# Optimization experiments

Hardware: AMD Instinct MI355X
Metric: run time of the kernel (lower is better)

The kernel has to match this reference:

```python
import jax, jax.numpy as jnp
import numpy as np

B, H, S, D = 2, 16, 2048, 64


def setup_inputs() -> dict:
    key = jax.random.key(0)
    kq, kk, kv = jax.random.split(key, 3)
    queries = jax.random.normal(kq, (B, H, S, D), dtype=jnp.float32)
    keys = jax.random.normal(kk, (B, H, S, D), dtype=jnp.float32)
    values = jax.random.normal(kv, (B, H, S, D), dtype=jnp.float32)
    scaling_factor = jnp.asarray(np.sqrt(D), dtype=jnp.float32)
    # causal mask, broadcast over heads: True = attend
    causal = jnp.tril(jnp.ones((S, S), dtype=bool))
    mask = jnp.broadcast_to(causal[None, None, :, :], (B, 1, S, S))
    return {
        "queries": queries,
        "keys": keys,
        "values": values,
        "scaling_factor": scaling_factor,
        "mask": mask,
    }


def reference(queries, keys, values, scaling_factor, mask):
    # scores: [B, H, S, S]
    scores = jnp.einsum("bhqd,bhkd->bhqk", queries, keys) / scaling_factor
    scores = jnp.where(mask, scores, -jnp.inf)
    attn = jax.nn.softmax(scores, axis=-1)
    # embeddings: [B, H, S, D]
    return jnp.einsum("bhqk,bhkd->bhqd", attn, values)
```

## Files before the change

### kernel.cpp

```cpp
#include <hip/hip_runtime.h>
#include <hip/hip_bf16.h>


typedef __attribute__((ext_vector_type(8))) short bf16x8;
typedef __attribute__((ext_vector_type(4))) float f32x4;
typedef unsigned uint2v __attribute__((ext_vector_type(2)));

#define MFMA32K(a, b, c) __builtin_amdgcn_mfma_f32_16x16x32_bf16(a, b, c, 0, 0, 0)

constexpr int Bsz = 2, Hn = 16, Sn = 2048, Dn = 64;
constexpr int QBLK = 64, KBLK = 64;
constexpr int NE = Bsz * Hn * Sn * Dn;

#if defined(__has_builtin)
#if __has_builtin(__builtin_amdgcn_exp2f)
#define EXP2(x) __builtin_amdgcn_exp2f(x)
#endif
#endif
#ifndef EXP2
#define EXP2(x) exp2f(x)
#endif

__device__ inline short f2bf(float f) {
  union { float f; unsigned u; } v;
  v.f = f;
  unsigned r = v.u + 0x7FFF + ((v.u >> 16) & 1);
  return (short)(r >> 16);
}

__device__ inline unsigned pk_bf16(float lo, float hi) {
  unsigned r;
  asm("v_cvt_pk_bf16_f32 %0, %1, %2" : "=v"(r) : "v"(lo), "v"(hi));
  return r;
}

__device__ inline void gl2lds16(const void* g, void* l) {
  __builtin_amdgcn_global_load_lds(
      (const __attribute__((address_space(1))) unsigned int*)g,
      (__attribute__((address_space(3))) unsigned int*)l, 16, 0, 0);
}

__device__ inline int swz(int row, int colbyte) {
  return row * 128 + (colbyte ^ ((row & 7) << 4));
}

#if defined(__has_builtin)
#if __has_builtin(__builtin_amdgcn_permlane16_swap) && \
    __has_builtin(__builtin_amdgcn_permlane32_swap)
#define HAVE_PERMLANE_SWAP 1
#endif
#endif

__device__ inline float xred_max(float x) {
#ifdef HAVE_PERMLANE_SWAP
  uint2v a = __builtin_amdgcn_permlane16_swap(__float_as_uint(x),
                                              __float_as_uint(x), false, false);
  x = fmaxf(__uint_as_float(a[0]), __uint_as_float(a[1]));
  uint2v b = __builtin_amdgcn_permlane32_swap(__float_as_uint(x),
                                              __float_as_uint(x), false, false);
  x = fmaxf(__uint_as_float(b[0]), __uint_as_float(b[1]));
#else
  x = fmaxf(x, __shfl_xor(x, 16, 64));
  x = fmaxf(x, __shfl_xor(x, 32, 64));
#endif
  return x;
}

__global__ __launch_bounds__(256) void prep(const float* __restrict__ K,
                                            const float* __restrict__ V,
                                            short* __restrict__ Kb,
                                            short* __restrict__ Vt) {
  const int tile = blockIdx.x, bh = blockIdx.y;
  const int tid = threadIdx.x;
  const int r = tid >> 2, c = (tid & 3) * 16;
  const size_t base = (size_t)bh * Sn * Dn;

  if (blockIdx.z == 0) {
    const float* kp = K + base + (size_t)(tile * 64 + r) * Dn + c;
    float4 x0 = *(const float4*)(kp + 0);
    float4 x1 = *(const float4*)(kp + 4);
    float4 x2 = *(const float4*)(kp + 8);
    float4 x3 = *(const float4*)(kp + 12);
    bf16x8 w0, w1;
    w0[0] = f2bf(x0.x); w0[1] = f2bf(x0.y); w0[2] = f2bf(x0.z); w0[3] = f2bf(x0.w);
    w0[4] = f2bf(x1.x); w0[5] = f2bf(x1.y); w0[6] = f2bf(x1.z); w0[7] = f2bf(x1.w);
    w1[0] = f2bf(x2.x); w1[1] = f2bf(x2.y); w1[2] = f2bf(x2.z); w1[3] = f2bf(x2.w);
    w1[4] = f2bf(x3.x); w1[5] = f2bf(x3.y); w1[6] = f2bf(x3.z); w1[7] = f2bf(x3.w);
    short* op = Kb + base + (size_t)(tile * 64 + r) * Dn + c;
    *(bf16x8*)op = w0;
    *(bf16x8*)(op + 8) = w1;
  } else {
    __shared__ short t[64][66];
    const float* vp = V + base + (size_t)(tile * 64 + r) * Dn + c;
    float4 x0 = *(const float4*)(vp + 0);
    float4 x1 = *(const float4*)(vp + 4);
    float4 x2 = *(const float4*)(vp + 8);
    float4 x3 = *(const float4*)(vp + 12);
    short* tr = &t[r][c];
    tr[0] = f2bf(x0.x); tr[1] = f2bf(x0.y); tr[2] = f2bf(x0.z); tr[3] = f2bf(x0.w);
    tr[4] = f2bf(x1.x); tr[5] = f2bf(x1.y); tr[6] = f2bf(x1.z); tr[7] = f2bf(x1.w);
    tr[8] = f2bf(x2.x); tr[9] = f2bf(x2.y); tr[10] = f2bf(x2.z); tr[11] = f2bf(x2.w);
    tr[12] = f2bf(x3.x); tr[13] = f2bf(x3.y); tr[14] = f2bf(x3.z); tr[15] = f2bf(x3.w);
    __syncthreads();
    short* op = Vt + base + (size_t)r * Sn + tile * 64 + c;
    bf16x8 w0, w1;
#pragma unroll
    for (int j = 0; j < 8; ++j) {
      int p0 = c + j, p1 = c + 8 + j;
      int k0 = 32 * (p0 >> 5) + 16 * ((p0 >> 2) & 1) + 4 * ((p0 >> 3) & 3) + (p0 & 3);
      int k1 = 32 * (p1 >> 5) + 16 * ((p1 >> 2) & 1) + 4 * ((p1 >> 3) & 3) + (p1 & 3);
      w0[j] = t[k0][r];
      w1[j] = t[k1][r];
    }
    *(bf16x8*)op = w0;
    *(bf16x8*)(op + 8) = w1;
  }
}

__global__ __launch_bounds__(256, 4) void attn_fwd(
    const float* __restrict__ Q, const short* __restrict__ Kb,
    const short* __restrict__ Vt, const float* __restrict__ SF,
    float* __restrict__ O) {
  __shared__ short Kbuf[2][64 * 64];
  __shared__ short Vbuf[2][64 * 64];

  const int bh = blockIdx.x;
  const int qt = (gridDim.y - 1) - blockIdx.y;
  const int tid = threadIdx.x;
  const int wave = tid >> 6, lane = tid & 63;
  const int g = lane >> 4, lc = lane & 15;
  const float qscale = 1.4426950408889634f / SF[0];

  const size_t base = (size_t)bh * Sn * Dn;
  const int qg = qt * QBLK + wave * 16 + lc;

  int ka[4][2], va[2][4];
#pragma unroll
  for (int t = 0; t < 4; ++t) {
    ka[t][0] = swz(t * 16 + lc, g * 16);
    ka[t][1] = swz(t * 16 + lc, g * 16 + 64);
  }
#pragma unroll
  for (int t2 = 0; t2 < 2; ++t2)
#pragma unroll
    for (int dt = 0; dt < 4; ++dt)
      va[t2][dt] = swz(dt * 16 + lc, t2 * 64 + g * 16);
  int koff[2], voff[2];
#pragma unroll
  for (int j = 0; j < 2; ++j) {
    int c = wave * 2 + j;
    int off = c * 1024 + lane * 16;
    int row = off >> 7;
    int col = (off & 127) ^ ((row & 7) << 4);
    koff[j] = row * 128 + col;
    voff[j] = row * (Sn * 2) + col;
  }

  const char* kpg = (const char*)(Kb + base);
  const char* vpg = (const char*)(Vt + base);

  auto stageK = [&](int buf) {
#pragma unroll
    for (int j = 0; j < 2; ++j)
      gl2lds16(kpg + koff[j], (char*)Kbuf[buf] + (wave * 2 + j) * 1024);
    kpg += KBLK * Dn * 2;
  };
  auto stageV = [&](int buf) {
#pragma unroll
    for (int j = 0; j < 2; ++j)
      gl2lds16(vpg + voff[j], (char*)Vbuf[buf] + (wave * 2 + j) * 1024);
    vpg += KBLK * 2;
  };

  bf16x8 bq[2];
  {
    const float* qp = Q + base + (size_t)qg * Dn + g * 8;
#pragma unroll
    for (int h = 0; h < 2; ++h) {
      float4 x0 = *(const float4*)(qp + 32 * h);
      float4 x1 = *(const float4*)(qp + 32 * h + 4);
      bf16x8 a;
      a[0] = f2bf(x0.x * qscale); a[1] = f2bf(x0.y * qscale);
      a[2] = f2bf(x0.z * qscale); a[3] = f2bf(x0.w * qscale);
      a[4] = f2bf(x1.x * qscale); a[5] = f2bf(x1.y * qscale);
      a[6] = f2bf(x1.z * qscale); a[7] = f2bf(x1.w * qscale);
      bq[h] = a;
    }
  }

  bf16x8 ones;
#pragma unroll
  for (int j = 0; j < 8; ++j) ones[j] = (short)0x3F80;

  f32x4 o[4], lsum = (f32x4){0.f, 0.f, 0.f, 0.f};
#pragma unroll
  for (int dt = 0; dt < 4; ++dt) o[dt] = (f32x4){0.f, 0.f, 0.f, 0.f};
  float m = -10000.0f;

  const int nt = qt + 1;
  int cur = 0;
  stageK(0);
  stageV(0);
  __syncthreads();

  for (int kt = 0; kt < nt; ++kt) {
    if (kt + 1 < nt) { stageK(cur ^ 1); stageV(cur ^ 1); }

    const char* Kc = (const char*)Kbuf[cur];
    const char* Vc = (const char*)Vbuf[cur];

    f32x4 s[4];
    __builtin_amdgcn_s_setprio(1);
#pragma unroll
    for (int t = 0; t < 4; ++t) {
      bf16x8 ak0 = *(const bf16x8*)(Kc + ka[t][0]);
      bf16x8 ak1 = *(const bf16x8*)(Kc + ka[t][1]);
      f32x4 z = (f32x4){0.f, 0.f, 0.f, 0.f};
      z = MFMA32K(ak0, bq[0], z);
      z = MFMA32K(ak1, bq[1], z);
      s[t] = z;
    }
    __builtin_amdgcn_s_setprio(0);

    if (kt == qt) {
      const int kb = kt * KBLK;
#pragma unroll
      for (int t = 0; t < 4; ++t)
#pragma unroll
        for (int i = 0; i < 4; ++i) {
          int kg = kb + t * 16 + g * 4 + i;
          if (kg > qg) s[t][i] = -30000.0f;
        }
    }

    float pmax = fmaxf(fmaxf(s[0][0], s[0][1]), fmaxf(s[0][2], s[0][3]));
#pragma unroll
    for (int t = 1; t < 4; ++t)
      pmax = fmaxf(pmax, fmaxf(fmaxf(s[t][0], s[t][1]),
                               fmaxf(s[t][2], s[t][3])));
    pmax = xred_max(pmax);
    if (!__all(pmax - m <= 8.0f)) {
      float mnew = fmaxf(m, pmax);
      float alpha = EXP2(m - mnew);
      lsum[0] *= alpha;
#pragma unroll
      for (int dt = 0; dt < 4; ++dt) o[dt] *= alpha;
      m = mnew;
    }
#pragma unroll
    for (int t = 0; t < 4; ++t)
#pragma unroll
      for (int i = 0; i < 4; ++i) s[t][i] = EXP2(s[t][i] - m);

    union { unsigned uu[4]; bf16x8 v; } pb[2];
#pragma unroll
    for (int t2 = 0; t2 < 2; ++t2) {
      pb[t2].uu[0] = pk_bf16(s[2 * t2][0], s[2 * t2][1]);
      pb[t2].uu[1] = pk_bf16(s[2 * t2][2], s[2 * t2][3]);
      pb[t2].uu[2] = pk_bf16(s[2 * t2 + 1][0], s[2 * t2 + 1][1]);
      pb[t2].uu[3] = pk_bf16(s[2 * t2 + 1][2], s[2 * t2 + 1][3]);
    }
    __builtin_amdgcn_s_setprio(1);
#pragma unroll
    for (int t2 = 0; t2 < 2; ++t2) {
      lsum = MFMA32K(ones, pb[t2].v, lsum);
#pragma unroll
      for (int dt = 0; dt < 4; ++dt) {
        bf16x8 av = *(const bf16x8*)(Vc + va[t2][dt]);
        o[dt] = MFMA32K(av, pb[t2].v, o[dt]);
      }
    }
    __builtin_amdgcn_s_setprio(0);

    __syncthreads();
    cur ^= 1;
  }

  const float inv = 1.0f / lsum[0];
  float* op = O + base + (size_t)qg * Dn;
#pragma unroll
  for (int dt = 0; dt < 4; ++dt) {
    f32x4 r = o[dt] * inv;
    *(f32x4*)(op + dt * 16 + g * 4) = r;
  }
}

extern "C" void kernel_launch(void* const* d_in, const int* in_sizes, int n_in,
                              void* d_out, int out_size, void* d_ws, size_t ws_size,
                              hipStream_t stream) {
  const float* Q = (const float*)d_in[0];
  const float* K = (const float*)d_in[1];
  const float* V = (const float*)d_in[2];
  const float* SF = (const float*)d_in[3];
  float* O = (float*)d_out;

  short* Kb = (short*)d_ws;
  short* Vt = Kb + NE;

  prep<<<dim3(Sn / 64, Bsz * Hn, 2), 256, 0, stream>>>(K, V, Kb, Vt);
  attn_fwd<<<dim3(Bsz * Hn, Sn / QBLK), 256, 0, stream>>>(Q, Kb, Vt, SF, O);
}
```

Before: 50.34 us.

## Pair causal query tiles per block and load V fragments directly from global

Each block now handles two query tiles (qt and 31-qt) one after the other, so every block does the same amount of causal work, and the grid is halved. V is no longer staged through LDS; each lane reads its V fragments straight from global memory into registers at the start of each iteration. Launch bounds drop to 2 blocks per CU, which allows more registers. The trade-off is fewer blocks in flight, global-latency V loads sitting on the critical path, and extra register pressure from holding the V fragments.

```diff
diff --git a/kernel.cpp b/kernel.cpp
--- a/kernel.cpp
+++ b/kernel.cpp
@@ -117,63 +117,51 @@
   }
 }
 
-__global__ __launch_bounds__(256, 4) void attn_fwd(
+__global__ __launch_bounds__(256, 2) void attn_fwd(
     const float* __restrict__ Q, const short* __restrict__ Kb,
     const short* __restrict__ Vt, const float* __restrict__ SF,
     float* __restrict__ O) {
   __shared__ short Kbuf[2][64 * 64];
-  __shared__ short Vbuf[2][64 * 64];
 
   const int bh = blockIdx.x;
-  const int qt = (gridDim.y - 1) - blockIdx.y;
+  const int py = blockIdx.y;
+  const int qtA = 31 - py, qtB = py;
+  const int nA = qtA + 1, nTot = nA + qtB + 1;
+
   const int tid = threadIdx.x;
   const int wave = tid >> 6, lane = tid & 63;
   const int g = lane >> 4, lc = lane & 15;
   const float qscale = 1.4426950408889634f / SF[0];
 
   const size_t base = (size_t)bh * Sn * Dn;
-  const int qg = qt * QBLK + wave * 16 + lc;
-
-  int ka[4][2], va[2][4];
+  const char* Kg = (const char*)(Kb + base);
+
+  int ka[4][2];
 #pragma unroll
   for (int t = 0; t < 4; ++t) {
     ka[t][0] = swz(t * 16 + lc, g * 16);
     ka[t][1] = swz(t * 16 + lc, g * 16 + 64);
   }
-#pragma unroll
-  for (int t2 = 0; t2 < 2; ++t2)
-#pragma unroll
-    for (int dt = 0; dt < 4; ++dt)
-      va[t2][dt] = swz(dt * 16 + lc, t2 * 64 + g * 16);
-  int koff[2], voff[2];
+  int koff[2];
 #pragma unroll
   for (int j = 0; j < 2; ++j) {
-    int c = wave * 2 + j;
-    int off = c * 1024 + lane * 16;
-    int row = off >> 7;
-    int col = (off & 127) ^ ((row & 7) << 4);
-    koff[j] = row * 128 + col;
-    voff[j] = row * (Sn * 2) + col;
-  }
-
-  const char* kpg = (const char*)(Kb + base);
-  const char* vpg = (const char*)(Vt + base);
-
-  auto stageK = [&](int buf) {
+    int c = (wave * 2 + j) * 1024 + lane * 16;
+    int row = c >> 7;
+    koff[j] = row * 128 + ((c & 127) ^ ((row & 7) << 4));
+  }
+  const char* vb[4];
+#pragma unroll
+  for (int dt = 0; dt < 4; ++dt)
+    vb[dt] = (const char*)(Vt + base) + (size_t)(dt * 16 + lc) * (Sn * 2) + g * 16;
+
+  auto stageK = [&](int kt, int buf) {
+    const char* src = Kg + ((size_t)kt << 13);
 #pragma unroll
     for (int j = 0; j < 2; ++j)
-      gl2lds16(kpg + koff[j], (char*)Kbuf[buf] + (wave * 2 + j) * 1024);
-    kpg += KBLK * Dn * 2;
+      gl2lds16(src + koff[j], (char*)Kbuf[buf] + (wave * 2 + j) * 1024);
   };
-  auto stageV = [&](int buf) {
-#pragma unroll
-    for (int j = 0; j < 2; ++j)
-      gl2lds16(vpg + voff[j], (char*)Vbuf[buf] + (wave * 2 + j) * 1024);
-    vpg += KBLK * 2;
-  };
-
-  bf16x8 bq[2];
-  {
+
+  auto loadQ = [&](int qg, bf16x8* bq) {
     const float* qp = Q + base + (size_t)qg * Dn + g * 8;
 #pragma unroll
     for (int h = 0; h < 2; ++h) {
@@ -186,28 +174,42 @@
       a[6] = f2bf(x1.z * qscale); a[7] = f2bf(x1.w * qscale);
       bq[h] = a;
     }
-  }
+  };
 
   bf16x8 ones;
 #pragma unroll
   for (int j = 0; j < 8; ++j) ones[j] = (short)0x3F80;
+
+  int qt = qtA;
+  int qg = qt * QBLK + wave * 16 + lc;
+  bf16x8 bq[2];
+  loadQ(qg, bq);
 
   f32x4 o[4], lsum = (f32x4){0.f, 0.f, 0.f, 0.f};
 #pragma unroll
   for (int dt = 0; dt < 4; ++dt) o[dt] = (f32x4){0.f, 0.f, 0.f, 0.f};
   float m = -10000.0f;
 
-  const int nt = qt + 1;
   int cur = 0;
-  stageK(0);
-  stageV(0);
+  stageK(0, 0);
   __syncthreads();
 
-  for (int kt = 0; kt < nt; ++kt) {
-    if (kt + 1 < nt) { stageK(cur ^ 1); stageV(cur ^ 1); }
+  for (int it = 0; it < nTot; ++it) {
+    const int kt = (it < nA) ? it : it - nA;
+
+    bf16x8 vf[2][4];
+#pragma unroll
+    for (int t2 = 0; t2 < 2; ++t2)
+#pragma unroll
+      for (int dt = 0; dt < 4; ++dt)
+        vf[t2][dt] = *(const bf16x8*)(vb[dt] + kt * 128 + t2 * 64);
+
+    if (it + 1 < nTot) {
+      int nkt = (it + 1 < nA) ? it + 1 : it + 1 - nA;
+      stageK(nkt, cur ^ 1);
+    }
 
     const char* Kc = (const char*)Kbuf[cur];
-    const char* Vc = (const char*)Vbuf[cur];
 
     f32x4 s[4];
     __builtin_amdgcn_s_setprio(1);
@@ -265,15 +267,30 @@
     for (int t2 = 0; t2 < 2; ++t2) {
       lsum = MFMA32K(ones, pb[t2].v, lsum);
 #pragma unroll
-      for (int dt = 0; dt < 4; ++dt) {
-        bf16x8 av = *(const bf16x8*)(Vc + va[t2][dt]);
-        o[dt] = MFMA32K(av, pb[t2].v, o[dt]);
-      }
+      for (int dt = 0; dt < 4; ++dt)
+        o[dt] = MFMA32K(vf[t2][dt], pb[t2].v, o[dt]);
     }
     __builtin_amdgcn_s_setprio(0);
 
     __syncthreads();
     cur ^= 1;
+
+    if (it == nA - 1) {
+      const float inv = 1.0f / lsum[0];
+      float* op = O + base + (size_t)qg * Dn;
+#pragma unroll
+      for (int dt = 0; dt < 4; ++dt) {
+        f32x4 r = o[dt] * inv;
+        *(f32x4*)(op + dt * 16 + g * 4) = r;
+      }
+      qt = qtB;
+      qg = qt * QBLK + wave * 16 + lc;
+      loadQ(qg, bq);
+#pragma unroll
+      for (int dt = 0; dt < 4; ++dt) o[dt] = (f32x4){0.f, 0.f, 0.f, 0.f};
+      lsum = (f32x4){0.f, 0.f, 0.f, 0.f};
+      m = -10000.0f;
+    }
   }
 
   const float inv = 1.0f / lsum[0];
@@ -298,5 +315,5 @@
   short* Vt = Kb + NE;
 
   prep<<<dim3(Sn / 64, Bsz * Hn, 2), 256, 0, stream>>>(K, V, Kb, Vt);
-  attn_fwd<<<dim3(Bsz * Hn, Sn / QBLK), 256, 0, stream>>>(Q, Kb, Vt, SF, O);
-}
+  attn_fwd<<<dim3(Bsz * Hn, 16), 256, 0, stream>>>(Q, Kb, Vt, SF, O);
+}
```

Result: slower. 81.99 us (+62.9%).

## Split KV tiles across wave pairs with 32-row queries per wave and merge

Applied to the files above, without the earlier changes.

Each attention block now gives every wave 32 query rows instead of 16, so each K/V fragment read from LDS feeds twice as many MFMAs. Waves are paired: one wave takes even KV tiles and the other takes odd tiles, and at the end the partial softmax states are merged through shared memory. The prep kernel now converts K and V in one block instead of two grid slices. In exchange, both LDS buffers hold different tiles at once, so each pair of tiles is loaded synchronously with two barriers and the overlap of loads with compute is lost. Register pressure also rises.

```diff
diff --git a/kernel.cpp b/kernel.cpp
--- a/kernel.cpp
+++ b/kernel.cpp
@@ -9,7 +9,7 @@
 #define MFMA32K(a, b, c) __builtin_amdgcn_mfma_f32_16x16x32_bf16(a, b, c, 0, 0, 0)
 
 constexpr int Bsz = 2, Hn = 16, Sn = 2048, Dn = 64;
-constexpr int QBLK = 64, KBLK = 64;
+constexpr int KBLK = 64;
 constexpr int NE = Bsz * Hn * Sn * Dn;
 
 #if defined(__has_builtin)
@@ -70,12 +70,13 @@
                                             const float* __restrict__ V,
                                             short* __restrict__ Kb,
                                             short* __restrict__ Vt) {
+  __shared__ short t[64][66];
   const int tile = blockIdx.x, bh = blockIdx.y;
   const int tid = threadIdx.x;
   const int r = tid >> 2, c = (tid & 3) * 16;
   const size_t base = (size_t)bh * Sn * Dn;
 
-  if (blockIdx.z == 0) {
+  {
     const float* kp = K + base + (size_t)(tile * 64 + r) * Dn + c;
     float4 x0 = *(const float4*)(kp + 0);
     float4 x1 = *(const float4*)(kp + 4);
@@ -89,8 +90,8 @@
     short* op = Kb + base + (size_t)(tile * 64 + r) * Dn + c;
     *(bf16x8*)op = w0;
     *(bf16x8*)(op + 8) = w1;
-  } else {
-    __shared__ short t[64][66];
+  }
+  {
     const float* vp = V + base + (size_t)(tile * 64 + r) * Dn + c;
     float4 x0 = *(const float4*)(vp + 0);
     float4 x1 = *(const float4*)(vp + 4);
@@ -128,11 +129,19 @@
   const int qt = (gridDim.y - 1) - blockIdx.y;
   const int tid = threadIdx.x;
   const int wave = tid >> 6, lane = tid & 63;
+  const int qh = wave >> 1, par = wave & 1;
   const int g = lane >> 4, lc = lane & 15;
   const float qscale = 1.4426950408889634f / SF[0];
 
   const size_t base = (size_t)bh * Sn * Dn;
-  const int qg = qt * QBLK + wave * 16 + lc;
+  const char* Kg = (const char*)(Kb + base);
+  const char* Vg = (const char*)(Vt + base);
+  const int nkv = qt + 1;
+  const int npairs = (nkv + 1) >> 1;
+
+  int qg[2];
+  qg[0] = qt * 64 + qh * 32 + lc;
+  qg[1] = qg[0] + 16;
 
   int ka[4][2], va[2][4];
 #pragma unroll
@@ -148,33 +157,30 @@
   int koff[2], voff[2];
 #pragma unroll
   for (int j = 0; j < 2; ++j) {
-    int c = wave * 2 + j;
-    int off = c * 1024 + lane * 16;
+    int off = (wave * 2 + j) * 1024 + lane * 16;
     int row = off >> 7;
     int col = (off & 127) ^ ((row & 7) << 4);
     koff[j] = row * 128 + col;
-    voff[j] = row * (Sn * 2) + col;
-  }
-
-  const char* kpg = (const char*)(Kb + base);
-  const char* vpg = (const char*)(Vt + base);
-
-  auto stageK = [&](int buf) {
+    voff[j] = row * 4096 + col;
+  }
+
+  auto stageK = [&](int kt, int buf) {
+    const char* src = Kg + (size_t)kt * 8192;
 #pragma unroll
     for (int j = 0; j < 2; ++j)
-      gl2lds16(kpg + koff[j], (char*)Kbuf[buf] + (wave * 2 + j) * 1024);
-    kpg += KBLK * Dn * 2;
+      gl2lds16(src + koff[j], (char*)Kbuf[buf] + (wave * 2 + j) * 1024);
   };
-  auto stageV = [&](int buf) {
+  auto stageV = [&](int kt, int buf) {
+    const char* src = Vg + (size_t)kt * 128;
 #pragma unroll
     for (int j = 0; j < 2; ++j)
-      gl2lds16(vpg + voff[j], (char*)Vbuf[buf] + (wave * 2 + j) * 1024);
-    vpg += KBLK * 2;
+      gl2lds16(src + voff[j], (char*)Vbuf[buf] + (wave * 2 + j) * 1024);
   };
 
-  bf16x8 bq[2];
-  {
-    const float* qp = Q + base + (size_t)qg * Dn + g * 8;
+  bf16x8 bq[2][2];
+#pragma unroll
+  for (int u = 0; u < 2; ++u) {
+    const float* qp = Q + base + (size_t)qg[u] * Dn + g * 8;
 #pragma unroll
     for (int h = 0; h < 2; ++h) {
       float4 x0 = *(const float4*)(qp + 32 * h);
@@ -184,7 +190,7 @@
       a[2] = f2bf(x0.z * qscale); a[3] = f2bf(x0.w * qscale);
       a[4] = f2bf(x1.x * qscale); a[5] = f2bf(x1.y * qscale);
       a[6] = f2bf(x1.z * qscale); a[7] = f2bf(x1.w * qscale);
-      bq[h] = a;
+      bq[u][h] = a;
     }
   }
 
@@ -192,96 +198,142 @@
 #pragma unroll
   for (int j = 0; j < 8; ++j) ones[j] = (short)0x3F80;
 
-  f32x4 o[4], lsum = (f32x4){0.f, 0.f, 0.f, 0.f};
-#pragma unroll
-  for (int dt = 0; dt < 4; ++dt) o[dt] = (f32x4){0.f, 0.f, 0.f, 0.f};
-  float m = -10000.0f;
-
-  const int nt = qt + 1;
-  int cur = 0;
-  stageK(0);
-  stageV(0);
+  f32x4 o[2][4], lsum[2];
+  float m[2] = {-10000.0f, -10000.0f};
+#pragma unroll
+  for (int u = 0; u < 2; ++u) {
+    lsum[u] = (f32x4){0.f, 0.f, 0.f, 0.f};
+#pragma unroll
+    for (int dt = 0; dt < 4; ++dt) o[u][dt] = (f32x4){0.f, 0.f, 0.f, 0.f};
+  }
+
+  stageK(0, 0);
+  stageV(0, 0);
+  if (nkv > 1) { stageK(1, 1); stageV(1, 1); }
   __syncthreads();
 
-  for (int kt = 0; kt < nt; ++kt) {
-    if (kt + 1 < nt) { stageK(cur ^ 1); stageV(cur ^ 1); }
-
-    const char* Kc = (const char*)Kbuf[cur];
-    const char* Vc = (const char*)Vbuf[cur];
-
-    f32x4 s[4];
-    __builtin_amdgcn_s_setprio(1);
-#pragma unroll
-    for (int t = 0; t < 4; ++t) {
-      bf16x8 ak0 = *(const bf16x8*)(Kc + ka[t][0]);
-      bf16x8 ak1 = *(const bf16x8*)(Kc + ka[t][1]);
-      f32x4 z = (f32x4){0.f, 0.f, 0.f, 0.f};
-      z = MFMA32K(ak0, bq[0], z);
-      z = MFMA32K(ak1, bq[1], z);
-      s[t] = z;
-    }
-    __builtin_amdgcn_s_setprio(0);
-
-    if (kt == qt) {
-      const int kb = kt * KBLK;
-#pragma unroll
-      for (int t = 0; t < 4; ++t)
-#pragma unroll
-        for (int i = 0; i < 4; ++i) {
-          int kg = kb + t * 16 + g * 4 + i;
-          if (kg > qg) s[t][i] = -30000.0f;
+  for (int j = 0; j < npairs; ++j) {
+    const int myt = 2 * j + par;
+    if (myt < nkv) {
+      const char* Kc = (const char*)Kbuf[par];
+      const char* Vc = (const char*)Vbuf[par];
+
+      f32x4 s[2][4];
+      __builtin_amdgcn_s_setprio(1);
+#pragma unroll
+      for (int t = 0; t < 4; ++t) {
+        bf16x8 ak0 = *(const bf16x8*)(Kc + ka[t][0]);
+        bf16x8 ak1 = *(const bf16x8*)(Kc + ka[t][1]);
+#pragma unroll
+        for (int u = 0; u < 2; ++u) {
+          f32x4 z = (f32x4){0.f, 0.f, 0.f, 0.f};
+          z = MFMA32K(ak0, bq[u][0], z);
+          z = MFMA32K(ak1, bq[u][1], z);
+          s[u][t] = z;
         }
-    }
-
-    float pmax = fmaxf(fmaxf(s[0][0], s[0][1]), fmaxf(s[0][2], s[0][3]));
-#pragma unroll
-    for (int t = 1; t < 4; ++t)
-      pmax = fmaxf(pmax, fmaxf(fmaxf(s[t][0], s[t][1]),
-                               fmaxf(s[t][2], s[t][3])));
-    pmax = xred_max(pmax);
-    if (!__all(pmax - m <= 8.0f)) {
-      float mnew = fmaxf(m, pmax);
-      float alpha = EXP2(m - mnew);
-      lsum[0] *= alpha;
-#pragma unroll
-      for (int dt = 0; dt < 4; ++dt) o[dt] *= alpha;
-      m = mnew;
-    }
-#pragma unroll
-    for (int t = 0; t < 4; ++t)
-#pragma unroll
-      for (int i = 0; i < 4; ++i) s[t][i] = EXP2(s[t][i] - m);
-
-    union { unsigned uu[4]; bf16x8 v; } pb[2];
-#pragma unroll
-    for (int t2 = 0; t2 < 2; ++t2) {
-      pb[t2].uu[0] = pk_bf16(s[2 * t2][0], s[2 * t2][1]);
-      pb[t2].uu[1] = pk_bf16(s[2 * t2][2], s[2 * t2][3]);
-      pb[t2].uu[2] = pk_bf16(s[2 * t2 + 1][0], s[2 * t2 + 1][1]);
-      pb[t2].uu[3] = pk_bf16(s[2 * t2 + 1][2], s[2 * t2 + 1][3]);
-    }
-    __builtin_amdgcn_s_setprio(1);
-#pragma unroll
-    for (int t2 = 0; t2 < 2; ++t2) {
-      lsum = MFMA32K(ones, pb[t2].v, lsum);
+      }
+      __builtin_amdgcn_s_setprio(0);
+
+      if (myt == qt) {
+        const int kb = myt * KBLK;
+#pragma unroll
+        for (int u = 0; u < 2; ++u)
+#pragma unroll
+          for (int t = 0; t < 4; ++t)
+#pragma unroll
+            for (int i = 0; i < 4; ++i) {
+              int kg = kb + t * 16 + g * 4 + i;
+              if (kg > qg[u]) s[u][t][i] = -30000.0f;
+            }
+      }
+
+      union { unsigned uu[4]; bf16x8 v; } pb[2][2];
+#pragma unroll
+      for (int u = 0; u < 2; ++u) {
+        float a0 = fmaxf(fmaxf(s[u][0][0], s[u][0][1]), s[u][0][2]);
+        float a1 = fmaxf(fmaxf(s[u][0][3], s[u][1][0]), s[u][1][1]);
+        float a2 = fmaxf(fmaxf(s[u][1][2], s[u][1][3]), s[u][2][0]);
+        float a3 = fmaxf(fmaxf(s[u][2][1], s[u][2][2]), s[u][2][3]);
+        float a4 = fmaxf(fmaxf(s[u][3][0], s[u][3][1]), s[u][3][2]);
+        float b0 = fmaxf(fmaxf(a0, a1), a2);
+        float b1 = fmaxf(fmaxf(a3, a4), s[u][3][3]);
+        float plocal = fmaxf(b0, b1);
+        if (!__all(plocal - m[u] <= 8.0f)) {
+          float pmax = xred_max(plocal);
+          float mnew = fmaxf(m[u], pmax);
+          float alpha = EXP2(m[u] - mnew);
+          lsum[u][0] *= alpha;
+#pragma unroll
+          for (int dt = 0; dt < 4; ++dt) o[u][dt] *= alpha;
+          m[u] = mnew;
+        }
+#pragma unroll
+        for (int t = 0; t < 4; ++t)
+#pragma unroll
+          for (int i = 0; i < 4; ++i) s[u][t][i] = EXP2(s[u][t][i] - m[u]);
+#pragma unroll
+        for (int t2 = 0; t2 < 2; ++t2) {
+          pb[u][t2].uu[0] = pk_bf16(s[u][2 * t2][0], s[u][2 * t2][1]);
+          pb[u][t2].uu[1] = pk_bf16(s[u][2 * t2][2], s[u][2 * t2][3]);
+          pb[u][t2].uu[2] = pk_bf16(s[u][2 * t2 + 1][0], s[u][2 * t2 + 1][1]);
+          pb[u][t2].uu[3] = pk_bf16(s[u][2 * t2 + 1][2], s[u][2 * t2 + 1][3]);
+        }
+      }
+
+      __builtin_amdgcn_s_setprio(1);
+#pragma unroll
+      for (int t2 = 0; t2 < 2; ++t2) {
+        lsum[0] = MFMA32K(ones, pb[0][t2].v, lsum[0]);
+        lsum[1] = MFMA32K(ones, pb[1][t2].v, lsum[1]);
+#pragma unroll
+        for (int dt = 0; dt < 4; ++dt) {
+          bf16x8 av = *(const bf16x8*)(Vc + va[t2][dt]);
+          o[0][dt] = MFMA32K(av, pb[0][t2].v, o[0][dt]);
+          o[1][dt] = MFMA32K(av, pb[1][t2].v, o[1][dt]);
+        }
+      }
+      __builtin_amdgcn_s_setprio(0);
+    }
+
+    __syncthreads();
+
+    const int nt0 = 2 * j + 2;
+    if (nt0 < nkv) { stageK(nt0, 0); stageV(nt0, 0); }
+    if (nt0 + 1 < nkv) { stageK(nt0 + 1, 1); stageV(nt0 + 1, 1); }
+    __syncthreads();
+  }
+
+  float* scr = (qh == 0) ? (float*)&Kbuf[0][0] : (float*)&Vbuf[0][0];
+  if (par == 1) {
+#pragma unroll
+    for (int u = 0; u < 2; ++u) {
+#pragma unroll
+      for (int dt = 0; dt < 4; ++dt)
+        *(f32x4*)(scr + (u * 16 + lc) * 64 + dt * 16 + g * 4) = o[u][dt];
+      if (g == 0) {
+        scr[2048 + u * 16 + lc] = m[u];
+        scr[2080 + u * 16 + lc] = lsum[u][0];
+      }
+    }
+  }
+  __syncthreads();
+  if (par == 0) {
+#pragma unroll
+    for (int u = 0; u < 2; ++u) {
+      float mB = scr[2048 + u * 16 + lc];
+      float lB = scr[2080 + u * 16 + lc];
+      float M = fmaxf(m[u], mB);
+      float aA = EXP2(m[u] - M), aB = EXP2(mB - M);
+      float inv = 1.0f / (lsum[u][0] * aA + lB * aB);
+      float cA = aA * inv, cB = aB * inv;
+      float* op = O + base + (size_t)qg[u] * Dn;
 #pragma unroll
       for (int dt = 0; dt < 4; ++dt) {
-        bf16x8 av = *(const bf16x8*)(Vc + va[t2][dt]);
-        o[dt] = MFMA32K(av, pb[t2].v, o[dt]);
-      }
-    }
-    __builtin_amdgcn_s_setprio(0);
-
-    __syncthreads();
-    cur ^= 1;
-  }
-
-  const float inv = 1.0f / lsum[0];
-  float* op = O + base + (size_t)qg * Dn;
-#pragma unroll
-  for (int dt = 0; dt < 4; ++dt) {
-    f32x4 r = o[dt] * inv;
-    *(f32x4*)(op + dt * 16 + g * 4) = r;
+        f32x4 oB = *(const f32x4*)(scr + (u * 16 + lc) * 64 + dt * 16 + g * 4);
+        f32x4 r = o[u][dt] * cA + oB * cB;
+        *(f32x4*)(op + dt * 16 + g * 4) = r;
+      }
+    }
   }
 }
 
@@ -297,6 +349,6 @@
   short* Kb = (short*)d_ws;
   short* Vt = Kb + NE;
 
-  prep<<<dim3(Sn / 64, Bsz * Hn, 2), 256, 0, stream>>>(K, V, Kb, Vt);
-  attn_fwd<<<dim3(Bsz * Hn, Sn / QBLK), 256, 0, stream>>>(Q, Kb, Vt, SF, O);
-}
+  prep<<<dim3(Sn / 64, Bsz * Hn), 256, 0, stream>>>(K, V, Kb, Vt);
+  attn_fwd<<<dim3(Bsz * Hn, Sn / 64), 256, 0, stream>>>(Q, Kb, Vt, SF, O);
+}
```

Result: faster. 44.39 us, median of 3 (-11.8%).
